# Optimization experiments

Hardware: AMD Instinct MI355X
Metric: run time of the kernel (lower is better)

## Reference

```python
import jax, jax.numpy as jnp
import numpy as np

N = 50000
E = 400000
IN_CH = 256
HEADS = 4
OUT_CH = 64
HID = HEADS * OUT_CH  # 256
ALPHA = 0.2
LN_EPS = 1e-5


def setup_inputs() -> dict:
    key = jax.random.key(0)
    ks = jax.random.split(key, 8)
    h = jax.random.normal(ks[0], (N, IN_CH), dtype=jnp.float32)
    edge_row = jax.random.randint(ks[1], (E,), 0, N, dtype=jnp.int32)
    edge_col = jax.random.randint(ks[2], (E,), 0, N, dtype=jnp.int32)
    # xavier-uniform-ish params
    def xavier(k, shape, fan_in, fan_out):
        lim = np.sqrt(6.0 / (fan_in + fan_out)).astype(np.float32)
        return jax.random.uniform(k, shape, jnp.float32, -lim, lim)
    W = xavier(ks[3], (IN_CH, HID), IN_CH, HID)              # Linear no bias
    attn_fc = xavier(ks[4], (HEADS, 2 * OUT_CH), 2 * OUT_CH, 1)
    ln_gamma = jnp.ones((HID,), jnp.float32)
    ln_beta = jnp.zeros((HID,), jnp.float32)
    ffn_w = xavier(ks[5], (HID, HID), HID, HID)
    ffn_b = jnp.zeros((HID,), jnp.float32)
    return {"h": h, "edge_row": edge_row, "edge_col": edge_col,
            "W": W, "attn_fc": attn_fc, "ln_gamma": ln_gamma,
            "ln_beta": ln_beta, "ffn_w": ffn_w, "ffn_b": ffn_b}


def reference(h, edge_row, edge_col, W, attn_fc, ln_gamma, ln_beta, ffn_w, ffn_b):
    # Wh: [N, H, D]
    Wh = (h @ W).reshape(N, HEADS, OUT_CH)
    Wh_i = Wh[edge_row]   # [E, H, D]
    Wh_j = Wh[edge_col]   # [E, H, D]
    # e = leakyrelu(cat(Wh_i, Wh_j) . attn_fc) per head -> split contraction
    a_src = attn_fc[:, :OUT_CH]  # [H, D]
    a_dst = attn_fc[:, OUT_CH:]  # [H, D]
    e = jnp.einsum('ehd,hd->eh', Wh_i, a_src) + jnp.einsum('ehd,hd->eh', Wh_j, a_dst)
    e = jax.nn.leaky_relu(e, negative_slope=ALPHA)
    # global max-shift exp (matches torch.exp(e - e.max(dim=0)))
    e = jnp.exp(e - jnp.max(e, axis=0, keepdims=True))  # [E, H]
    e_sum = jax.ops.segment_sum(e, edge_row, num_segments=N)  # [N, H]
    alpha = e / (e_sum[edge_row] + 1e-15)  # [E, H]  (dropout = identity in eval)
    # scatter-add weighted messages
    h_new = jax.ops.segment_sum(Wh_j * alpha[..., None], edge_row, num_segments=N)
    h_new = h_new.reshape(N, HID) + Wh.reshape(N, HID)  # residual (shapes match)
    # LayerNorm
    mu = jnp.mean(h_new, axis=-1, keepdims=True)
    var = jnp.var(h_new, axis=-1, keepdims=True)
    h_new = (h_new - mu) * jax.lax.rsqrt(var + LN_EPS) * ln_gamma + ln_beta
    # FFN: Linear + ReLU (+ dropout identity)
    return jax.nn.relu(h_new @ ffn_w + ffn_b)
```

## Files before the change

### kernel.cpp

```cpp
#include <hip/hip_runtime.h>
#include <hip/hip_bf16.h>

#define N_NODES 50000
#define E_EDGES 400000
#define IN_CH   256
#define HEADS   4
#define OUT_CH  64
#define HID     256
#define ALPHA   0.2f
#define LN_EPS  1e-5f

using f32x16 = __attribute__((ext_vector_type(16))) float;
using bf16x8 = __attribute__((ext_vector_type(8))) short;
using u16x8  = __attribute__((ext_vector_type(8))) unsigned short;
using u16x4  = __attribute__((ext_vector_type(4))) unsigned short;

typedef __attribute__((address_space(3))) void* lds_vp;
typedef const __attribute__((address_space(1))) void* gbl_vp;

__device__ __forceinline__ unsigned short f2bf(float f) {
    __hip_bfloat16 b = __float2bfloat16(f);
    return *(unsigned short*)&b;
}
__device__ __forceinline__ float bf2f(unsigned short u) {
    __hip_bfloat16 b = *(__hip_bfloat16*)&u;
    return __bfloat162float(b);
}

__global__ __launch_bounds__(256) void prep_kernel(
    const float* __restrict__ W, const float* __restrict__ ffn_w,
    unsigned short* __restrict__ Wt, unsigned short* __restrict__ Ft)
{
    int i = blockIdx.x * 256 + threadIdx.x;
    if (i < 65536) {
        int n = i >> 8, k = i & 255;
        Wt[i] = f2bf(W[k * 256 + n]);
    } else {
        int j = i - 65536;
        int n = j >> 8, k = j & 255;
        Ft[j] = f2bf(ffn_w[k * 256 + n]);
    }
}

template<bool A_IS_F32, bool RELU_BIAS>
__global__ __launch_bounds__(512, 4) void gemm_bres(
    const void* __restrict__ Av, const unsigned short* __restrict__ Bt,
    const float* __restrict__ bias, void* __restrict__ Cv, int M)
{
    __shared__ unsigned short Bs[128 * 256];

    const int tid = threadIdx.x;
    const int lane = tid & 63, wid = tid >> 6;
    const int colhalf = blockIdx.x & 1;
    const int col0 = colhalf * 128;
    const int sb = blockIdx.x >> 1;

    #pragma unroll
    for (int i = 0; i < 8; i++) {
        int d = i * 512 + tid;
        int n = d >> 5, cp = d & 31;
        int cs = cp ^ (n & 31);
        const unsigned short* g = Bt + (size_t)(col0 + n) * 256 + cs * 8;
        __builtin_amdgcn_global_load_lds((gbl_vp)g, (lds_vp)&Bs[(size_t)d * 8],
                                         16, 0, 0);
    }
    __syncthreads();

    const int strip = wid * 256 + sb;
    const int r0 = strip * 32;
    if (r0 >= M) return;

    const int q5 = lane & 31, kg = lane >> 5;
    const int rowc = min(r0 + q5, M - 1);

    f32x16 acc[4] = {};

    const float* Af = (const float*)Av;
    const unsigned short* Ab = (const unsigned short*)Av;

    float4 pa[2], pb[2]; u16x8 pc[2];
    auto loadA = [&](int t, int slot) {
        if (A_IS_F32) {
            const float* p = Af + (size_t)rowc * 256 + t * 16 + kg * 8;
            pa[slot] = *(const float4*)p; pb[slot] = *(const float4*)(p + 4);
        } else {
            pc[slot] = *(const u16x8*)(Ab + (size_t)rowc * 256 + t * 16 + kg * 8);
        }
    };
    loadA(0, 0); loadA(1, 1);

    #pragma unroll
    for (int t = 0; t < 16; t++) {
        const int slot = t & 1;
        bf16x8 af;
        if (A_IS_F32) {
            union { unsigned int u[4]; bf16x8 v; } cv;
            cv.u[0] = (unsigned)f2bf(pa[slot].x) | ((unsigned)f2bf(pa[slot].y) << 16);
            cv.u[1] = (unsigned)f2bf(pa[slot].z) | ((unsigned)f2bf(pa[slot].w) << 16);
            cv.u[2] = (unsigned)f2bf(pb[slot].x) | ((unsigned)f2bf(pb[slot].y) << 16);
            cv.u[3] = (unsigned)f2bf(pb[slot].z) | ((unsigned)f2bf(pb[slot].w) << 16);
            af = cv.v;
        } else {
            union { u16x8 u; bf16x8 v; } cv; cv.u = pc[slot]; af = cv.v;
        }
        if (t + 2 < 16) loadA(t + 2, slot);
        #pragma unroll
        for (int n = 0; n < 4; n++) {
            const bf16x8 bf = *(const bf16x8*)((const char*)Bs +
                (size_t)(n * 32 + q5) * 512 + (((t * 2 + kg) ^ q5) * 16));
            acc[n] = __builtin_amdgcn_mfma_f32_32x32x16_bf16(af, bf, acc[n], 0, 0, 0);
        }
    }

    #pragma unroll
    for (int n = 0; n < 4; n++) {
        int gc = col0 + n * 32 + q5;
        float bv = RELU_BIAS ? bias[gc] : 0.f;
        #pragma unroll
        for (int reg = 0; reg < 16; reg++) {
            int rl = (reg & 3) + 8 * (reg >> 2) + 4 * kg;
            int gr = r0 + rl;
            if (gr >= M) continue;
            float v = acc[n][reg];
            if (RELU_BIAS) {
                v += bv; v = v > 0.f ? v : 0.f;
                ((float*)Cv)[(size_t)gr * 256 + gc] = v;
            } else {
                ((unsigned short*)Cv)[(size_t)gr * 256 + gc] = f2bf(v);
            }
        }
    }
}

__global__ __launch_bounds__(256) void scores_kernel(
    const unsigned short* __restrict__ Wh, const float* __restrict__ attn_fc,
    float* __restrict__ s_src, float* __restrict__ s_dst)
{
    const int lane = threadIdx.x & 63, wid = threadIdx.x >> 6;
    const int n = blockIdx.x * 4 + wid;
    const int h = lane >> 4;
    const int d0 = 4 * (lane & 15);
    u16x4 w = *(const u16x4*)(Wh + (size_t)n * HID + 4 * lane);
    float ps = 0.f, pd = 0.f;
    #pragma unroll
    for (int q = 0; q < 4; q++) {
        float wf = bf2f(w[q]);
        ps += wf * attn_fc[h * 128 + d0 + q];
        pd += wf * attn_fc[h * 128 + 64 + d0 + q];
    }
    #pragma unroll
    for (int off = 8; off; off >>= 1) {
        ps += __shfl_xor(ps, off, 16);
        pd += __shfl_xor(pd, off, 16);
    }
    if ((lane & 15) == 0) {
        s_src[n * HEADS + h] = ps;
        s_dst[n * HEADS + h] = pd;
    }
}

__global__ void hist_kernel(const int* __restrict__ erow, int* __restrict__ counts) {
    int e = blockIdx.x * blockDim.x + threadIdx.x;
    if (e < E_EDGES) atomicAdd(&counts[erow[e]], 1);
}

__global__ __launch_bounds__(256) void scanA_kernel(
    const int* __restrict__ counts, int* __restrict__ bsum)
{
    const int b = blockIdx.x, tid = threadIdx.x;
    int i0 = b * 512 + tid;
    int v = 0;
    if (i0 < N_NODES) v += counts[i0];
    if (i0 + 256 < N_NODES) v += counts[i0 + 256];
    #pragma unroll
    for (int off = 32; off; off >>= 1) v += __shfl_xor(v, off, 64);
    __shared__ int ws[4];
    if ((tid & 63) == 0) ws[tid >> 6] = v;
    __syncthreads();
    if (tid == 0) bsum[b] = ws[0] + ws[1] + ws[2] + ws[3];
}

__global__ __launch_bounds__(128) void scanB_kernel(
    const int* __restrict__ bsum, int* __restrict__ bscan, int nb)
{
    const int tid = threadIdx.x;
    const int lane = tid & 63, wid = tid >> 6;
    int val = (tid < nb) ? bsum[tid] : 0;
    int x = val;
    #pragma unroll
    for (int off = 1; off < 64; off <<= 1) {
        int y = __shfl_up(x, off, 64);
        if (lane >= off) x += y;
    }
    __shared__ int w0;
    if (tid == 63) w0 = x;
    __syncthreads();
    if (wid == 1) x += w0;
    if (tid < nb) bscan[tid] = x - val;
}

__global__ __launch_bounds__(512) void scanC_kernel(
    const int* __restrict__ counts, const int* __restrict__ bscan,
    int* __restrict__ offsets, int* __restrict__ cursor)
{
    const int b = blockIdx.x, tid = threadIdx.x;
    const int lane = tid & 63, wid = tid >> 6;
    const int i = b * 512 + tid;
    int v = (i < N_NODES) ? counts[i] : 0;
    int x = v;
    #pragma unroll
    for (int off = 1; off < 64; off <<= 1) {
        int y = __shfl_up(x, off, 64);
        if (lane >= off) x += y;
    }
    __shared__ int ws[8];
    if (lane == 63) ws[wid] = x;
    __syncthreads();
    if (wid == 0 && lane < 8) {
        int s = ws[lane];
        #pragma unroll
        for (int off = 1; off < 8; off <<= 1) {
            int y = __shfl_up(s, off, 8);
            if ((lane & 7) >= off) s += y;
        }
        ws[lane] = s;
    }
    __syncthreads();
    int prefix = (wid ? ws[wid - 1] : 0) + bscan[b];
    int excl = prefix + x - v;
    if (i < N_NODES) { offsets[i] = excl; cursor[i] = excl; }
    if (i == N_NODES - 1) offsets[N_NODES] = excl + v;
}

__global__ __launch_bounds__(256) void scatter_kernel(
    const int* __restrict__ erow, const int* __restrict__ ecol,
    const float* __restrict__ s_src, const float* __restrict__ s_dst,
    int* __restrict__ cursor, int* __restrict__ sorted_col,
    float4* __restrict__ sorted_w)
{
    int e = blockIdx.x * blockDim.x + threadIdx.x;
    if (e >= E_EDGES) return;
    int r = erow[e], c = ecol[e];
    float4 ss = ((const float4*)s_src)[r];
    float4 sd = ((const float4*)s_dst)[c];
    float sc[4] = {ss.x + sd.x, ss.y + sd.y, ss.z + sd.z, ss.w + sd.w};
    float4 w;
    float* wp = (float*)&w;
    #pragma unroll
    for (int h = 0; h < 4; h++) {
        float v = sc[h] > 0.f ? sc[h] : ALPHA * sc[h];
        wp[h] = __expf(v);
    }
    int pos = atomicAdd(&cursor[r], 1);
    sorted_col[pos] = c;
    sorted_w[pos] = w;
}

__global__ __launch_bounds__(256) void aggregate_ln_kernel(
    const unsigned short* __restrict__ Wh, const float* __restrict__ sorted_w,
    const int* __restrict__ offsets, const int* __restrict__ sorted_col,
    const float* __restrict__ ln_gamma, const float* __restrict__ ln_beta,
    unsigned short* __restrict__ h_ln)
{
    const int lane = threadIdx.x & 63, wid = threadIdx.x >> 6;
    const int n = blockIdx.x * 4 + wid;
    const int p = lane >> 5;
    const int q5 = lane & 31;
    const int c0 = q5 * 8;
    const int h = q5 >> 3;
    const int beg = offsets[n], end = offsets[n + 1];

    float acc[8] = {};
    float wsum = 0.f;
    for (int base = beg; base < end; base += 64) {
        int cnt = min(64, end - base);
        int cv = (base + lane < end) ? sorted_col[base + lane] : 0;
        int jj = 0;
        #pragma unroll 2
        for (; jj + 2 <= cnt; jj += 2) {
            int c = __shfl(cv, jj + p, 64);
            float w = sorted_w[(size_t)(base + jj + p) * 4 + h];
            u16x8 r = *(const u16x8*)(Wh + (size_t)c * HID + c0);
            wsum += w;
            #pragma unroll
            for (int k = 0; k < 8; k++) acc[k] += w * bf2f(r[k]);
        }
        if (jj < cnt) {
            int c = __shfl(cv, jj, 64);
            if (p == 0) {
                float w = sorted_w[(size_t)(base + jj) * 4 + h];
                u16x8 r = *(const u16x8*)(Wh + (size_t)c * HID + c0);
                wsum += w;
                #pragma unroll
                for (int k = 0; k < 8; k++) acc[k] += w * bf2f(r[k]);
            }
        }
    }
    wsum += __shfl_xor(wsum, 32, 64);
    #pragma unroll
    for (int k = 0; k < 8; k++) acc[k] += __shfl_xor(acc[k], 32, 64);

    u16x8 rr = *(const u16x8*)(Wh + (size_t)n * HID + c0);
    float inv_w = 1.f / (wsum + 1e-15f);
    float val[8];
    float s = 0.f;
    #pragma unroll
    for (int k = 0; k < 8; k++) {
        val[k] = acc[k] * inv_w + bf2f(rr[k]);
        s += val[k];
    }
    #pragma unroll
    for (int off = 16; off; off >>= 1) s += __shfl_xor(s, off, 64);
    float mu = s * (1.f / HID);
    float s2 = 0.f;
    #pragma unroll
    for (int k = 0; k < 8; k++) { float d = val[k] - mu; s2 += d * d; }
    #pragma unroll
    for (int off = 16; off; off >>= 1) s2 += __shfl_xor(s2, off, 64);
    float inv_std = rsqrtf(s2 * (1.f / HID) + LN_EPS);

    if (p == 0) {
        float4 g0 = *(const float4*)(ln_gamma + c0);
        float4 g1 = *(const float4*)(ln_gamma + c0 + 4);
        float4 b0 = *(const float4*)(ln_beta + c0);
        float4 b1 = *(const float4*)(ln_beta + c0 + 4);
        u16x8 outv;
        outv[0] = f2bf((val[0] - mu) * inv_std * g0.x + b0.x);
        outv[1] = f2bf((val[1] - mu) * inv_std * g0.y + b0.y);
        outv[2] = f2bf((val[2] - mu) * inv_std * g0.z + b0.z);
        outv[3] = f2bf((val[3] - mu) * inv_std * g0.w + b0.w);
        outv[4] = f2bf((val[4] - mu) * inv_std * g1.x + b1.x);
        outv[5] = f2bf((val[5] - mu) * inv_std * g1.y + b1.y);
        outv[6] = f2bf((val[6] - mu) * inv_std * g1.z + b1.z);
        outv[7] = f2bf((val[7] - mu) * inv_std * g1.w + b1.w);
        *(u16x8*)(h_ln + (size_t)n * HID + c0) = outv;
    }
}

extern "C" void kernel_launch(void* const* d_in, const int* in_sizes, int n_in,
                              void* d_out, int out_size, void* d_ws, size_t ws_size,
                              hipStream_t stream)
{
    const float* h        = (const float*)d_in[0];
    const int*   erow     = (const int*)  d_in[1];
    const int*   ecol     = (const int*)  d_in[2];
    const float* W        = (const float*)d_in[3];
    const float* attn_fc  = (const float*)d_in[4];
    const float* ln_gamma = (const float*)d_in[5];
    const float* ln_beta  = (const float*)d_in[6];
    const float* ffn_w    = (const float*)d_in[7];
    const float* ffn_b    = (const float*)d_in[8];
    float* out = (float*)d_out;

    unsigned short* Wh   = (unsigned short*)d_ws;
    unsigned short* h_ln = Wh + (size_t)N_NODES * HID;
    unsigned short* Wt   = h_ln + (size_t)N_NODES * HID;
    unsigned short* Ft   = Wt + 65536;
    float* s_src  = (float*)(Ft + 65536);
    float* s_dst  = s_src + N_NODES * HEADS;
    float* sorted_w = s_dst + N_NODES * HEADS;
    int*   counts = (int*)(sorted_w + (size_t)E_EDGES * HEADS);
    int*   offsets = counts + N_NODES;
    int*   cursor  = offsets + N_NODES + 1;
    int*   sorted_col = cursor + N_NODES;
    int*   bsum   = sorted_col + E_EDGES;
    int*   bscan  = bsum + 128;

    const int NB = (N_NODES + 511) / 512;

    hipMemsetAsync(counts, 0, N_NODES * sizeof(int), stream);
    prep_kernel<<<512, 256, 0, stream>>>(W, ffn_w, Wt, Ft);

    gemm_bres<true, false><<<512, 512, 0, stream>>>(h, Wt, nullptr, Wh, N_NODES);

    scores_kernel<<<N_NODES / 4, 256, 0, stream>>>(Wh, attn_fc, s_src, s_dst);
    hist_kernel<<<(E_EDGES + 255) / 256, 256, 0, stream>>>(erow, counts);
    scanA_kernel<<<NB, 256, 0, stream>>>(counts, bsum);
    scanB_kernel<<<1, 128, 0, stream>>>(bsum, bscan, NB);
    scanC_kernel<<<NB, 512, 0, stream>>>(counts, bscan, offsets, cursor);
    scatter_kernel<<<(E_EDGES + 255) / 256, 256, 0, stream>>>(
        erow, ecol, s_src, s_dst, cursor, sorted_col, (float4*)sorted_w);
    aggregate_ln_kernel<<<N_NODES / 4, 256, 0, stream>>>(
        Wh, sorted_w, offsets, sorted_col, ln_gamma, ln_beta, h_ln);

    gemm_bres<false, true><<<512, 512, 0, stream>>>(h_ln, Ft, ffn_b, out, N_NODES);
}
```

Baseline: 249.8 us.

## Stage bf16 GEMM output through LDS for vectorized stores; remap block order

For the bf16-output GEMM, accumulator tiles are written to the shared-memory B buffer and then stored to global memory as 16-byte row-contiguous vectors. This replaces scattered 2-byte stores. Block indexing is changed so consecutive blocks share the same column half rather than alternating between halves. The early return is replaced with an active flag so every thread reaches the added barriers, at the cost of two extra syncs and an LDS round trip.

```diff
diff --git a/kernel.cpp b/kernel.cpp
--- a/kernel.cpp
+++ b/kernel.cpp
@@ -51,9 +51,9 @@
 
     const int tid = threadIdx.x;
     const int lane = tid & 63, wid = tid >> 6;
-    const int colhalf = blockIdx.x & 1;
+    const int colhalf = blockIdx.x >> 8;
     const int col0 = colhalf * 128;
-    const int sb = blockIdx.x >> 1;
+    const int sb = blockIdx.x & 255;
 
     #pragma unroll
     for (int i = 0; i < 8; i++) {
@@ -68,10 +68,10 @@
 
     const int strip = wid * 256 + sb;
     const int r0 = strip * 32;
-    if (r0 >= M) return;
+    const bool active = (r0 < M);
 
     const int q5 = lane & 31, kg = lane >> 5;
-    const int rowc = min(r0 + q5, M - 1);
+    const int rowc = active ? min(r0 + q5, M - 1) : 0;
 
     f32x16 acc[4] = {};
 
@@ -87,46 +87,73 @@
             pc[slot] = *(const u16x8*)(Ab + (size_t)rowc * 256 + t * 16 + kg * 8);
         }
     };
-    loadA(0, 0); loadA(1, 1);
-
-    #pragma unroll
-    for (int t = 0; t < 16; t++) {
-        const int slot = t & 1;
-        bf16x8 af;
-        if (A_IS_F32) {
-            union { unsigned int u[4]; bf16x8 v; } cv;
-            cv.u[0] = (unsigned)f2bf(pa[slot].x) | ((unsigned)f2bf(pa[slot].y) << 16);
-            cv.u[1] = (unsigned)f2bf(pa[slot].z) | ((unsigned)f2bf(pa[slot].w) << 16);
-            cv.u[2] = (unsigned)f2bf(pb[slot].x) | ((unsigned)f2bf(pb[slot].y) << 16);
-            cv.u[3] = (unsigned)f2bf(pb[slot].z) | ((unsigned)f2bf(pb[slot].w) << 16);
-            af = cv.v;
-        } else {
-            union { u16x8 u; bf16x8 v; } cv; cv.u = pc[slot]; af = cv.v;
-        }
-        if (t + 2 < 16) loadA(t + 2, slot);
+
+    if (active) {
+        loadA(0, 0); loadA(1, 1);
         #pragma unroll
-        for (int n = 0; n < 4; n++) {
-            const bf16x8 bf = *(const bf16x8*)((const char*)Bs +
-                (size_t)(n * 32 + q5) * 512 + (((t * 2 + kg) ^ q5) * 16));
-            acc[n] = __builtin_amdgcn_mfma_f32_32x32x16_bf16(af, bf, acc[n], 0, 0, 0);
-        }
-    }
-
-    #pragma unroll
-    for (int n = 0; n < 4; n++) {
-        int gc = col0 + n * 32 + q5;
-        float bv = RELU_BIAS ? bias[gc] : 0.f;
-        #pragma unroll
-        for (int reg = 0; reg < 16; reg++) {
-            int rl = (reg & 3) + 8 * (reg >> 2) + 4 * kg;
-            int gr = r0 + rl;
-            if (gr >= M) continue;
-            float v = acc[n][reg];
-            if (RELU_BIAS) {
-                v += bv; v = v > 0.f ? v : 0.f;
-                ((float*)Cv)[(size_t)gr * 256 + gc] = v;
+        for (int t = 0; t < 16; t++) {
+            const int slot = t & 1;
+            bf16x8 af;
+            if (A_IS_F32) {
+                union { unsigned int u[4]; bf16x8 v; } cv;
+                cv.u[0] = (unsigned)f2bf(pa[slot].x) | ((unsigned)f2bf(pa[slot].y) << 16);
+                cv.u[1] = (unsigned)f2bf(pa[slot].z) | ((unsigned)f2bf(pa[slot].w) << 16);
+                cv.u[2] = (unsigned)f2bf(pb[slot].x) | ((unsigned)f2bf(pb[slot].y) << 16);
+                cv.u[3] = (unsigned)f2bf(pb[slot].z) | ((unsigned)f2bf(pb[slot].w) << 16);
+                af = cv.v;
             } else {
-                ((unsigned short*)Cv)[(size_t)gr * 256 + gc] = f2bf(v);
+                union { u16x8 u; bf16x8 v; } cv; cv.u = pc[slot]; af = cv.v;
+            }
+            if (t + 2 < 16) loadA(t + 2, slot);
+            #pragma unroll
+            for (int n = 0; n < 4; n++) {
+                const bf16x8 bf = *(const bf16x8*)((const char*)Bs +
+                    (size_t)(n * 32 + q5) * 512 + (((t * 2 + kg) ^ q5) * 16));
+                acc[n] = __builtin_amdgcn_mfma_f32_32x32x16_bf16(af, bf, acc[n], 0, 0, 0);
+            }
+        }
+    }
+
+    if (RELU_BIAS) {
+        if (active) {
+            #pragma unroll
+            for (int n = 0; n < 4; n++) {
+                int gc = col0 + n * 32 + q5;
+                float bv = bias[gc];
+                #pragma unroll
+                for (int reg = 0; reg < 16; reg++) {
+                    int rl = (reg & 3) + 8 * (reg >> 2) + 4 * kg;
+                    int gr = r0 + rl;
+                    if (gr >= M) continue;
+                    float v = acc[n][reg] + bv;
+                    v = v > 0.f ? v : 0.f;
+                    ((float*)Cv)[(size_t)gr * 256 + gc] = v;
+                }
+            }
+        }
+    } else {
+        __syncthreads();
+        unsigned short* T = Bs + wid * 4096;
+        if (active) {
+            #pragma unroll
+            for (int n = 0; n < 4; n++) {
+                #pragma unroll
+                for (int reg = 0; reg < 16; reg++) {
+                    int rl = (reg & 3) + 8 * (reg >> 2) + 4 * kg;
+                    T[rl * 128 + n * 32 + q5] = f2bf(acc[n][reg]);
+                }
+            }
+        }
+        __syncthreads();
+        if (active) {
+            #pragma unroll
+            for (int i = 0; i < 8; i++) {
+                int row = i * 4 + (lane >> 4);
+                int cb = (lane & 15) * 8;
+                u16x8 v = *(const u16x8*)(T + row * 128 + cb);
+                int gr = r0 + row;
+                if (gr < M)
+                    *(u16x8*)((unsigned short*)Cv + (size_t)gr * 256 + col0 + cb) = v;
             }
         }
     }
```

New measurement: 248.4 us. About the same (-0.6%).
